# Performance work log

Hardware: AMD Instinct MI355X
Metric: run time of the kernel (lower is better)

The kernel has to match this reference:

```python
import jax, jax.numpy as jnp
import numpy as np
import math

B, S, HID = 2, 2048, 512
H, HKV, QB, VB = 8, 2, 8, 16
W = 256 // QB            # suffix window size = 32
QKD = W * QB             # unfolded qk dim = 256
TAU = 1.0


def setup_inputs() -> dict:
    key = jax.random.key(0)
    ks = jax.random.split(key, 7)
    return {
        "hidden_states": jax.random.normal(ks[0], (B, S, HID), jnp.float32),
        "Wq": jax.random.normal(ks[1], (H * QB, HID), jnp.float32) * (HID ** -0.5),
        "Wk": jax.random.normal(ks[2], (HKV * QB, HID), jnp.float32) * (HID ** -0.5),
        "Wv": jax.random.normal(ks[3], (HKV * VB, HID), jnp.float32) * (HID ** -0.5),
        "Wo": jax.random.normal(ks[4], (HID, H * VB), jnp.float32) * ((H * VB) ** -0.5),
        "v_emb0": jnp.full((H * VB,), -1e-5, jnp.float32),
        "v_emb1": jnp.full((H * VB,), +1e-5, jnp.float32),
    }


def _forward(hidden_states, Wq, Wk, Wv, Wo, v_emb0, v_emb1):
    b, s, _ = hidden_states.shape
    # bit-quantized (soft) q/k/v projections
    q = jnp.tanh((hidden_states @ Wq.T) / TAU).reshape(b, s, H, QB).transpose(0, 2, 1, 3)      # [B,H,S,QB]
    k = jnp.tanh((hidden_states @ Wk.T) / TAU).reshape(b, s, HKV, QB).transpose(0, 2, 1, 3)    # [B,HKV,S,QB]
    v = jax.nn.sigmoid((hidden_states @ Wv.T) / TAU).reshape(b, s, HKV, VB).transpose(0, 2, 1, 3)
    # suffix shift of values: F.pad(v, (0,0,-1,1)) -> v[t] <- v[t+1], last position zero
    v = jnp.concatenate([v[:, :, 1:], jnp.zeros_like(v[:, :, :1])], axis=2)                    # [B,HKV,S,VB]
    # left-pad seq by W-1 zeros, then unfold sliding windows of length W
    pad = ((0, 0), (0, 0), (W - 1, 0), (0, 0))
    qp, kp = jnp.pad(q, pad), jnp.pad(k, pad)
    win = jnp.arange(s)[:, None] + jnp.arange(W)[None, :]   # [S,W] window indices into padded seq
    qw = qp[:, :, win, :].reshape(b, H, s, QKD)             # concat window positions x bits
    kw = kp[:, :, win, :].reshape(b, HKV, s, QKD)
    # GQA: repeat kv heads
    rep = H // HKV
    kw = jnp.repeat(kw, rep, axis=1)
    vr = jnp.repeat(v, rep, axis=1)
    scale = 1.0 / math.sqrt(QKD) / TAU
    # custom bias r_j / (r_i + 1) under strictly-causal mask (j < i)
    r = jnp.arange(s, dtype=hidden_states.dtype)
    mask = jnp.tril(jnp.ones((s, s), dtype=bool), -1)
    bias = jnp.where(mask, (r[None, :] / (r[:, None] + 1.0)) / TAU, 0.0)
    scores = jnp.einsum('bhqd,bhkd->bhqk', qw, kw) * scale + bias
    neg = jnp.finfo(scores.dtype).min
    scores = jnp.where(mask, scores, neg)
    # stable masked softmax (fully-masked row 0 -> zero weights instead of NaN)
    scores = scores - jax.lax.stop_gradient(jnp.max(scores, axis=-1, keepdims=True))
    e = jnp.exp(scores) * mask
    attn = e / jnp.maximum(jnp.sum(e, axis=-1, keepdims=True), 1e-30)
    out = jnp.einsum('bhqk,bhkd->bhqd', attn, vr)           # [B,H,S,VB]
    out = out.transpose(0, 2, 1, 3).reshape(b, s, H * VB)
    # learned emb0/emb1 interpolation
    out = out * v_emb1 + (1.0 - out) * v_emb0
    return out @ Wo.T


def reference(hidden_states, Wq, Wk, Wv, Wo, v_emb0, v_emb1):
    return _forward(hidden_states, Wq, Wk, Wv, Wo, v_emb0, v_emb1)
```

## Files before the change

### kernel.cpp

```cpp
#include <hip/hip_runtime.h>
#include <hip/hip_bf16.h>

typedef unsigned int u32;
typedef unsigned short u16;
typedef float f32x4 __attribute__((ext_vector_type(4)));
typedef short s16x8 __attribute__((ext_vector_type(8)));

#define B_   2
#define S_   2048
#define HID_ 512
#define H_   8
#define HKV_ 2
#define QB_  8
#define VB_  16
#define NQ_  64
#define HVB_ 128
#define LOG2E_ 1.4426950408889634f
#define MFIX2_ 24.525815695089866f

__device__ __forceinline__ u16 f2bf(float f) {
    u32 b = __builtin_bit_cast(u32, f);
    b += 0x7FFFu + ((b >> 16) & 1u);
    return (u16)(b >> 16);
}
__device__ __forceinline__ u16 bf16u(float f) {
    return __builtin_bit_cast(u16, (__bf16)f);
}
__device__ __forceinline__ f32x4 mfma16(s16x8 a, s16x8 b, f32x4 c) {
    return __builtin_amdgcn_mfma_f32_16x16x32_bf16(a, b, c, 0, 0, 0);
}
__device__ __forceinline__ float fast_tanh(float x) {
    float e = exp2f(x * (2.f * LOG2E_));
    return 1.f - 2.f * __builtin_amdgcn_rcpf(e + 1.f);
}
__device__ __forceinline__ float fast_sigmoid(float x) {
    return __builtin_amdgcn_rcpf(1.f + exp2f(-LOG2E_ * x));
}

__global__ void k0_convert(const float* __restrict__ Wq, const float* __restrict__ Wk,
                           const float* __restrict__ Wv, const float* __restrict__ Wo,
                           u16* __restrict__ Wc, u16* __restrict__ Wob) {
    int idx = blockIdx.x * 256 + threadIdx.x;
    {
        int n = idx >> 9, k = idx & 511;
        float v = (n < NQ_) ? Wq[n * HID_ + k]
                : (n < NQ_ + 16) ? Wk[(n - NQ_) * HID_ + k]
                : (n < 112) ? Wv[(n - NQ_ - 16) * HID_ + k] : 0.f;
        Wc[idx] = f2bf(v);
    }
    Wob[idx] = f2bf(Wo[idx]);
}

__global__ __launch_bounds__(256) void k1_proj(
    const float* __restrict__ hidden, const u16* __restrict__ Wc,
    u16* __restrict__ qb, u16* __restrict__ kb, u16* __restrict__ vt)
{
    const int tid = threadIdx.x;
    const int r0 = blockIdx.x * 16;
    const int wv = tid >> 6, lane = tid & 63;
    const int li = lane & 15, lo4 = lane >> 4;

    const float* hrow = hidden + (r0 + li) * HID_;

    f32x4 acc[2];
    acc[0] = (f32x4){0.f, 0.f, 0.f, 0.f};
    acc[1] = (f32x4){0.f, 0.f, 0.f, 0.f};

    #pragma unroll
    for (int kc = 0; kc < 16; ++kc) {
        f32x4 x0 = *(const f32x4*)&hrow[32 * kc + 8 * lo4];
        f32x4 x1 = *(const f32x4*)&hrow[32 * kc + 8 * lo4 + 4];
        s16x8 a = { (short)f2bf(x0[0]), (short)f2bf(x0[1]), (short)f2bf(x0[2]), (short)f2bf(x0[3]),
                    (short)f2bf(x1[0]), (short)f2bf(x1[1]), (short)f2bf(x1[2]), (short)f2bf(x1[3]) };
        #pragma unroll
        for (int u = 0; u < 2; ++u) {
            int n = (wv + 4 * u) * 16 + li;
            s16x8 bfr = *(const s16x8*)&Wc[n * HID_ + 32 * kc + 8 * lo4];
            acc[u] = mfma16(a, bfr, acc[u]);
        }
    }

    #pragma unroll
    for (int u = 0; u < 2; ++u) {
        int n = (wv + 4 * u) * 16 + li;
        if (n < 112) {
            #pragma unroll
            for (int reg = 0; reg < 4; ++reg) {
                int gs = r0 + 4 * lo4 + reg;
                int b = gs >> 11, s = gs & 2047;
                float pre = acc[u][reg];
                if (n < NQ_) {
                    int h = n >> 3, bit = n & 7;
                    qb[(((b * H_ + h) * S_) + s) * QB_ + bit] =
                        f2bf(fast_tanh(pre) * (0.0625f * LOG2E_));
                } else if (n < NQ_ + 16) {
                    int nk = n - NQ_;
                    kb[(((b * HKV_ + (nk >> 3)) * S_) + s) * QB_ + (nk & 7)] = f2bf(fast_tanh(pre));
                } else {
                    int nv = n - NQ_ - 16;
                    int hv = nv >> 4, vb = nv & 15;
                    u16 sig = f2bf(fast_sigmoid(pre));
                    if (s > 0)
                        vt[((b * HKV_ + hv) * VB_ + vb) * S_ + (s - 1)] = sig;
                    if (s == S_ - 1)
                        vt[((b * HKV_ + hv) * VB_ + vb) * S_ + (S_ - 1)] = 0;
                }
            }
        }
    }
}

__global__ __launch_bounds__(256, 2) void k2_attn(
    const u16* __restrict__ qb, const u16* __restrict__ kb, const u16* __restrict__ vt,
    const float* __restrict__ vemb0, const float* __restrict__ vemb1,
    u16* __restrict__ AO)
{
    __shared__ __align__(16) u16 psa[4][32 * 72];
    __shared__ float Om[4][2][16][16];
    __shared__ float lv[4][2][16];

    const int bid = blockIdx.x;
    const int rb = bid >> 4;
    const int r  = (rb < 32) ? (63 - rb) : (rb - 32);
    const int I0 = r * 32;
    const int nJ = ((I0 + 30) >> 6) + 1;
    const int bh = bid & 15;
    const int b = bh >> 3, h = bh & 7, hkv = h >> 2;

    const int g = threadIdx.x >> 6;
    const int lane = threadIdx.x & 63;
    const int li = lane & 15, lo4 = lane >> 4;

    u16* psw = psa[g];
    const u16* kpl = kb + ((b * HKV_ + hkv) * S_) * QB_ + (li + lo4 - 31) * QB_;
    const u16* vtp = vt + ((b * HKV_ + hkv) * VB_) * S_ + li * S_ + 8 * lo4;

    s16x8 qf[2][8];
    #pragma unroll
    for (int ig = 0; ig < 2; ++ig) {
        const int gr0 = I0 + 16 * ig + li - 31 + lo4;
        const u16* qp = qb + ((b * H_ + h) * S_) * QB_ + gr0 * QB_;
        #pragma unroll
        for (int kk = 0; kk < 8; ++kk) {
            s16x8 v = {0, 0, 0, 0, 0, 0, 0, 0};
            if (gr0 + 4 * kk >= 0) v = *(const s16x8*)(qp + kk * 32);
            qf[ig][kk] = v;
        }
    }

    int ibase[2];
    float binv[2][4];
    #pragma unroll
    for (int ig = 0; ig < 2; ++ig) {
        ibase[ig] = I0 + 16 * ig + 4 * lo4;
        #pragma unroll
        for (int reg = 0; reg < 4; ++reg) {
            float d = (float)(ibase[ig] + reg + 1);
            float rc = __builtin_amdgcn_rcpf(d);
            rc = rc * (2.f - d * rc);
            binv[ig][reg] = rc * LOG2E_;
        }
    }

    f32x4 O[2];
    O[0] = (f32x4){0.f, 0.f, 0.f, 0.f};
    O[1] = (f32x4){0.f, 0.f, 0.f, 0.f};
    float lsum[2][4] = {{0.f, 0.f, 0.f, 0.f}, {0.f, 0.f, 0.f, 0.f}};

    s16x8 ld[20];
    {
        const u16* kt = kpl + g * 512;
        if (g == 0) {
            #pragma unroll
            for (int m = 0; m < 20; ++m) {
                s16x8 v = {0, 0, 0, 0, 0, 0, 0, 0};
                if (li + lo4 + 4 * m >= 31) v = *(const s16x8*)(kt + 32 * m);
                ld[m] = v;
            }
        } else {
            #pragma unroll
            for (int m = 0; m < 20; ++m)
                ld[m] = *(const s16x8*)(kt + 32 * m);
        }
    }

    for (int jt = g; jt < nJ; jt += 4) {
        const int J0 = jt * 64;

        s16x8 vfr0 = *(const s16x8*)(vtp + J0);
        s16x8 vfr1 = *(const s16x8*)(vtp + J0 + 32);

        f32x4 sacc[2][4];
        #pragma unroll
        for (int ig = 0; ig < 2; ++ig)
            #pragma unroll
            for (int ns = 0; ns < 4; ++ns)
                sacc[ig][ns] = (f32x4){0.f, 0.f, 0.f, 0.f};
        #pragma unroll
        for (int m = 0; m < 20; ++m) {
            s16x8 f = ld[m];
            {
                int kk = m & 3, ns = m >> 2;
                if (ns < 4) {
                    sacc[0][ns] = mfma16(qf[0][kk], f, sacc[0][ns]);
                    sacc[1][ns] = mfma16(qf[1][kk], f, sacc[1][ns]);
                }
            }
            {
                int kk = (m & 3) + 4, ns = (m >> 2) - 1;
                if (ns >= 0) {
                    sacc[0][ns] = mfma16(qf[0][kk], f, sacc[0][ns]);
                    sacc[1][ns] = mfma16(qf[1][kk], f, sacc[1][ns]);
                }
            }
        }

        if (jt + 4 < nJ) {
            const u16* kt = kpl + (jt + 4) * 512;
            #pragma unroll
            for (int m = 0; m < 20; ++m)
                ld[m] = *(const s16x8*)(kt + 32 * m);
        }

        const float jlif = (float)(J0 + li);
        #pragma unroll
        for (int ig = 0; ig < 2; ++ig) {
            const bool edgev = (J0 + 63) >= (I0 + 16 * ig);
            #pragma unroll
            for (int reg = 0; reg < 4; ++reg) {
                const int irow = ibase[ig] + reg;
                const float bi = binv[ig][reg];
                float p[4];
                #pragma unroll
                for (int ns = 0; ns < 4; ++ns) {
                    float bns = fmaf(jlif + (float)(16 * ns), bi, -MFIX2_);
                    float e = exp2f(sacc[ig][ns][reg] + bns);
                    if (edgev)
                        e = (J0 + 16 * ns + li < irow) ? e : 0.f;
                    p[ns] = e;
                }
                lsum[ig][reg] += (p[0] + p[1]) + (p[2] + p[3]);
                #pragma unroll
                for (int ns = 0; ns < 4; ++ns)
                    psw[(ig * 16 + 4 * lo4 + reg) * 72 + 16 * ns + li] = bf16u(p[ns]);
            }
        }

        #pragma unroll
        for (int ig = 0; ig < 2; ++ig) {
            s16x8 pa0 = *(const s16x8*)&psw[(ig * 16 + li) * 72 + 8 * lo4];
            s16x8 pa1 = *(const s16x8*)&psw[(ig * 16 + li) * 72 + 32 + 8 * lo4];
            O[ig] = mfma16(pa0, vfr0, O[ig]);
            O[ig] = mfma16(pa1, vfr1, O[ig]);
        }
    }

    #pragma unroll
    for (int ig = 0; ig < 2; ++ig) {
        #pragma unroll
        for (int reg = 0; reg < 4; ++reg) {
            float l = lsum[ig][reg];
            l += __shfl_xor(l, 1);
            l += __shfl_xor(l, 2);
            l += __shfl_xor(l, 4);
            l += __shfl_xor(l, 8);
            Om[g][ig][4 * lo4 + reg][li] = O[ig][reg];
            if (li == 0) lv[g][ig][4 * lo4 + reg] = l;
        }
    }
    __syncthreads();

    if (g == 0) {
        const int hc = h * VB_ + li;
        const float e0 = vemb0[hc], e1 = vemb1[hc];
        #pragma unroll
        for (int ig = 0; ig < 2; ++ig) {
            #pragma unroll
            for (int reg = 0; reg < 4; ++reg) {
                const int row = 4 * lo4 + reg;
                float Oc = (Om[0][ig][row][li] + Om[1][ig][row][li])
                         + (Om[2][ig][row][li] + Om[3][ig][row][li]);
                float lc = (lv[0][ig][row] + lv[1][ig][row])
                         + (lv[2][ig][row] + lv[3][ig][row]);
                float lr = fmaxf(lc, 1e-30f);
                float rinv = __builtin_amdgcn_rcpf(lr);
                rinv = rinv * (2.f - lr * rinv);
                float o = Oc * rinv;
                const int s = I0 + 16 * ig + row;
                AO[(b * S_ + s) * HVB_ + hc] = f2bf(e0 + o * (e1 - e0));
            }
        }
    }
}

__global__ __launch_bounds__(256) void k3_out(
    const u16* __restrict__ AO, const u16* __restrict__ Wob,
    float* __restrict__ out)
{
    const int tid = threadIdx.x;
    const int r0 = (blockIdx.x >> 2) * 16;
    const int cg = blockIdx.x & 3;
    const int wv = tid >> 6, lane = tid & 63;
    const int li = lane & 15, lo4 = lane >> 4;

    const u16* arow = AO + (r0 + li) * HVB_;

    f32x4 acc[2];
    acc[0] = (f32x4){0.f, 0.f, 0.f, 0.f};
    acc[1] = (f32x4){0.f, 0.f, 0.f, 0.f};

    #pragma unroll
    for (int kc = 0; kc < 4; ++kc) {
        s16x8 a = *(const s16x8*)&arow[32 * kc + 8 * lo4];
        #pragma unroll
        for (int u = 0; u < 2; ++u) {
            int o = cg * 128 + (wv + 4 * u) * 16 + li;
            s16x8 bfr = *(const s16x8*)&Wob[o * HVB_ + 32 * kc + 8 * lo4];
            acc[u] = mfma16(a, bfr, acc[u]);
        }
    }

    #pragma unroll
    for (int u = 0; u < 2; ++u) {
        int o = cg * 128 + (wv + 4 * u) * 16 + li;
        #pragma unroll
        for (int reg = 0; reg < 4; ++reg)
            out[(r0 + 4 * lo4 + reg) * HID_ + o] = acc[u][reg];
    }
}

extern "C" void kernel_launch(void* const* d_in, const int* in_sizes, int n_in,
                              void* d_out, int out_size, void* d_ws, size_t ws_size,
                              hipStream_t stream)
{
    (void)in_sizes; (void)n_in; (void)out_size;
    const float* hidden = (const float*)d_in[0];
    const float* Wq = (const float*)d_in[1];
    const float* Wk = (const float*)d_in[2];
    const float* Wv = (const float*)d_in[3];
    const float* Wo = (const float*)d_in[4];
    const float* ve0 = (const float*)d_in[5];
    const float* ve1 = (const float*)d_in[6];
    float* out = (float*)d_out;

    char* base = (char*)d_ws;
    u16* qb  = (u16*)(base);
    u16* kb  = (u16*)(base + 524288);
    u16* vt  = (u16*)(base + 655360);
    u16* AO  = (u16*)(base + 917504);
    u16* Wc  = (u16*)(base + 1966080);
    u16* Wob = (u16*)(base + 2097152);
    if (ws_size < 2228224) return;

    hipLaunchKernelGGL(k0_convert, dim3(256), dim3(256), 0, stream,
                       Wq, Wk, Wv, Wo, Wc, Wob);
    hipLaunchKernelGGL(k1_proj, dim3(256), dim3(256), 0, stream,
                       hidden, Wc, qb, kb, vt);
    hipLaunchKernelGGL(k2_attn, dim3(1024), dim3(256), 0, stream,
                       qb, kb, vt, ve0, ve1, AO);
    hipLaunchKernelGGL(k3_out, dim3(1024), dim3(256), 0, stream,
                       AO, Wob, out);
}
```

Baseline: 62.90 us.

## Share overlapping Q fragments, use hardware bf16 convert, add MFMA priority hints

The manual round-to-nearest bf16 conversion is replaced everywhere with the compiler's native __bf16 cast. In the attention kernel, the two query row groups (16 rows apart) share overlapping window fragments, so 12 fragment registers replace 16, which cuts register pressure and global loads. The change also precomputes the LDS write and read addresses for the P tile, makes the bias term incremental instead of recomputed per column, interleaves the PV MFMA per row group, and wraps the MFMA sections in s_setprio. These are several small, mostly independent tweaks whose effect on a largely latency-bound kernel is uncertain.

```diff
diff --git a/kernel.cpp b/kernel.cpp
--- a/kernel.cpp
+++ b/kernel.cpp
@@ -18,11 +18,6 @@
 #define LOG2E_ 1.4426950408889634f
 #define MFIX2_ 24.525815695089866f
 
-__device__ __forceinline__ u16 f2bf(float f) {
-    u32 b = __builtin_bit_cast(u32, f);
-    b += 0x7FFFu + ((b >> 16) & 1u);
-    return (u16)(b >> 16);
-}
 __device__ __forceinline__ u16 bf16u(float f) {
     return __builtin_bit_cast(u16, (__bf16)f);
 }
@@ -46,9 +41,9 @@
         float v = (n < NQ_) ? Wq[n * HID_ + k]
                 : (n < NQ_ + 16) ? Wk[(n - NQ_) * HID_ + k]
                 : (n < 112) ? Wv[(n - NQ_ - 16) * HID_ + k] : 0.f;
-        Wc[idx] = f2bf(v);
-    }
-    Wob[idx] = f2bf(Wo[idx]);
+        Wc[idx] = bf16u(v);
+    }
+    Wob[idx] = bf16u(Wo[idx]);
 }
 
 __global__ __launch_bounds__(256) void k1_proj(
@@ -70,8 +65,8 @@
     for (int kc = 0; kc < 16; ++kc) {
         f32x4 x0 = *(const f32x4*)&hrow[32 * kc + 8 * lo4];
         f32x4 x1 = *(const f32x4*)&hrow[32 * kc + 8 * lo4 + 4];
-        s16x8 a = { (short)f2bf(x0[0]), (short)f2bf(x0[1]), (short)f2bf(x0[2]), (short)f2bf(x0[3]),
-                    (short)f2bf(x1[0]), (short)f2bf(x1[1]), (short)f2bf(x1[2]), (short)f2bf(x1[3]) };
+        s16x8 a = { (short)bf16u(x0[0]), (short)bf16u(x0[1]), (short)bf16u(x0[2]), (short)bf16u(x0[3]),
+                    (short)bf16u(x1[0]), (short)bf16u(x1[1]), (short)bf16u(x1[2]), (short)bf16u(x1[3]) };
         #pragma unroll
         for (int u = 0; u < 2; ++u) {
             int n = (wv + 4 * u) * 16 + li;
@@ -92,14 +87,14 @@
                 if (n < NQ_) {
                     int h = n >> 3, bit = n & 7;
                     qb[(((b * H_ + h) * S_) + s) * QB_ + bit] =
-                        f2bf(fast_tanh(pre) * (0.0625f * LOG2E_));
+                        bf16u(fast_tanh(pre) * (0.0625f * LOG2E_));
                 } else if (n < NQ_ + 16) {
                     int nk = n - NQ_;
-                    kb[(((b * HKV_ + (nk >> 3)) * S_) + s) * QB_ + (nk & 7)] = f2bf(fast_tanh(pre));
+                    kb[(((b * HKV_ + (nk >> 3)) * S_) + s) * QB_ + (nk & 7)] = bf16u(fast_tanh(pre));
                 } else {
                     int nv = n - NQ_ - 16;
                     int hv = nv >> 4, vb = nv & 15;
-                    u16 sig = f2bf(fast_sigmoid(pre));
+                    u16 sig = bf16u(fast_sigmoid(pre));
                     if (s > 0)
                         vt[((b * HKV_ + hv) * VB_ + vb) * S_ + (s - 1)] = sig;
                     if (s == S_ - 1)
@@ -135,21 +130,30 @@
     const u16* kpl = kb + ((b * HKV_ + hkv) * S_) * QB_ + (li + lo4 - 31) * QB_;
     const u16* vtp = vt + ((b * HKV_ + hkv) * VB_) * S_ + li * S_ + 8 * lo4;
 
-    s16x8 qf[2][8];
+    u16* wadr[2][4];
+    const u16* radr[2];
     #pragma unroll
     for (int ig = 0; ig < 2; ++ig) {
-        const int gr0 = I0 + 16 * ig + li - 31 + lo4;
+        #pragma unroll
+        for (int reg = 0; reg < 4; ++reg)
+            wadr[ig][reg] = psw + (ig * 16 + 4 * lo4 + reg) * 72 + li;
+        radr[ig] = psw + (ig * 16 + li) * 72 + 8 * lo4;
+    }
+
+    s16x8 qfu[12];
+    {
+        const int gr0 = I0 + li - 31 + lo4;
         const u16* qp = qb + ((b * H_ + h) * S_) * QB_ + gr0 * QB_;
         #pragma unroll
-        for (int kk = 0; kk < 8; ++kk) {
+        for (int m = 0; m < 12; ++m) {
             s16x8 v = {0, 0, 0, 0, 0, 0, 0, 0};
-            if (gr0 + 4 * kk >= 0) v = *(const s16x8*)(qp + kk * 32);
-            qf[ig][kk] = v;
+            if (gr0 + 4 * m >= 0) v = *(const s16x8*)(qp + m * 32);
+            qfu[m] = v;
         }
     }
 
     int ibase[2];
-    float binv[2][4];
+    float binv[2][4], bstep[2][4];
     #pragma unroll
     for (int ig = 0; ig < 2; ++ig) {
         ibase[ig] = I0 + 16 * ig + 4 * lo4;
@@ -159,6 +163,7 @@
             float rc = __builtin_amdgcn_rcpf(d);
             rc = rc * (2.f - d * rc);
             binv[ig][reg] = rc * LOG2E_;
+            bstep[ig][reg] = 16.f * rc * LOG2E_;
         }
     }
 
@@ -196,24 +201,26 @@
             #pragma unroll
             for (int ns = 0; ns < 4; ++ns)
                 sacc[ig][ns] = (f32x4){0.f, 0.f, 0.f, 0.f};
+        __builtin_amdgcn_s_setprio(1);
         #pragma unroll
         for (int m = 0; m < 20; ++m) {
             s16x8 f = ld[m];
             {
                 int kk = m & 3, ns = m >> 2;
                 if (ns < 4) {
-                    sacc[0][ns] = mfma16(qf[0][kk], f, sacc[0][ns]);
-                    sacc[1][ns] = mfma16(qf[1][kk], f, sacc[1][ns]);
+                    sacc[0][ns] = mfma16(qfu[kk],     f, sacc[0][ns]);
+                    sacc[1][ns] = mfma16(qfu[kk + 4], f, sacc[1][ns]);
                 }
             }
             {
                 int kk = (m & 3) + 4, ns = (m >> 2) - 1;
                 if (ns >= 0) {
-                    sacc[0][ns] = mfma16(qf[0][kk], f, sacc[0][ns]);
-                    sacc[1][ns] = mfma16(qf[1][kk], f, sacc[1][ns]);
+                    sacc[0][ns] = mfma16(qfu[kk],     f, sacc[0][ns]);
+                    sacc[1][ns] = mfma16(qfu[kk + 4], f, sacc[1][ns]);
                 }
             }
         }
+        __builtin_amdgcn_s_setprio(0);
 
         if (jt + 4 < nJ) {
             const u16* kt = kpl + (jt + 4) * 512;
@@ -229,29 +236,28 @@
             #pragma unroll
             for (int reg = 0; reg < 4; ++reg) {
                 const int irow = ibase[ig] + reg;
-                const float bi = binv[ig][reg];
+                float bns = fmaf(jlif, binv[ig][reg], -MFIX2_);
                 float p[4];
                 #pragma unroll
                 for (int ns = 0; ns < 4; ++ns) {
-                    float bns = fmaf(jlif + (float)(16 * ns), bi, -MFIX2_);
                     float e = exp2f(sacc[ig][ns][reg] + bns);
+                    bns += bstep[ig][reg];
                     if (edgev)
                         e = (J0 + 16 * ns + li < irow) ? e : 0.f;
                     p[ns] = e;
                 }
                 lsum[ig][reg] += (p[0] + p[1]) + (p[2] + p[3]);
-                #pragma unroll
-                for (int ns = 0; ns < 4; ++ns)
-                    psw[(ig * 16 + 4 * lo4 + reg) * 72 + 16 * ns + li] = bf16u(p[ns]);
-            }
-        }
-
-        #pragma unroll
-        for (int ig = 0; ig < 2; ++ig) {
-            s16x8 pa0 = *(const s16x8*)&psw[(ig * 16 + li) * 72 + 8 * lo4];
-            s16x8 pa1 = *(const s16x8*)&psw[(ig * 16 + li) * 72 + 32 + 8 * lo4];
+                wadr[ig][reg][0]  = bf16u(p[0]);
+                wadr[ig][reg][16] = bf16u(p[1]);
+                wadr[ig][reg][32] = bf16u(p[2]);
+                wadr[ig][reg][48] = bf16u(p[3]);
+            }
+            s16x8 pa0 = *(const s16x8*)(radr[ig]);
+            s16x8 pa1 = *(const s16x8*)(radr[ig] + 32);
+            __builtin_amdgcn_s_setprio(1);
             O[ig] = mfma16(pa0, vfr0, O[ig]);
             O[ig] = mfma16(pa1, vfr1, O[ig]);
+            __builtin_amdgcn_s_setprio(0);
         }
     }
 
@@ -287,7 +293,7 @@
                 rinv = rinv * (2.f - lr * rinv);
                 float o = Oc * rinv;
                 const int s = I0 + 16 * ig + row;
-                AO[(b * S_ + s) * HVB_ + hc] = f2bf(e0 + o * (e1 - e0));
+                AO[(b * S_ + s) * HVB_ + hc] = bf16u(e0 + o * (e1 - e0));
             }
         }
     }
@@ -298,7 +304,7 @@
     float* __restrict__ out)
 {
     const int tid = threadIdx.x;
-    const int r0 = (blockIdx.x >> 2) * 16;
+    const int r0 = (int)(blockIdx.x >> 2) * 16;
     const int cg = blockIdx.x & 3;
     const int wv = tid >> 6, lane = tid & 63;
     const int li = lane & 15, lo4 = lane >> 4;
```

Result: slower. 65.03 us (+3.4%).
